# Kernel tuning notes

Measured on AMD Instinct MI355X. Metric: run time of the kernel, lower is better.

The kernel has to match this reference:

```python
import jax, jax.numpy as jnp
import numpy as np

B, T, D, E, FF, K = 4, 1024, 1024, 8, 2048, 2
SINKHORN_ITERS = 3


def setup_inputs() -> dict:
    key = jax.random.key(0)
    ks = jax.random.split(key, 7)
    scale = 0.02
    return {
        "x": jax.random.normal(ks[0], (B, T, D), dtype=jnp.float32),
        "router_w": jax.random.normal(ks[1], (E, D), dtype=jnp.float32) * scale,  # nn.Linear(D,E).weight
        "router_b": jnp.zeros((E,), dtype=jnp.float32),
        "temperature": jnp.ones((1,), dtype=jnp.float32) * 0.5,
        "wg": jax.random.normal(ks[2], (E, D, FF), dtype=jnp.float32) * scale,   # expert gate weights
        "wp": jax.random.normal(ks[3], (E, D, FF), dtype=jnp.float32) * scale,   # expert proj weights
        "wo": jax.random.normal(ks[4], (E, FF, D), dtype=jnp.float32) * scale,   # expert out_proj weights
    }


def _sinkhorn(log_alpha, iters=SINKHORN_ITERS):
    for _ in range(iters):
        log_alpha = log_alpha - jax.nn.logsumexp(log_alpha, axis=-1, keepdims=True)
        log_alpha = log_alpha - jax.nn.logsumexp(log_alpha, axis=-2, keepdims=True)
    gates = jnp.exp(log_alpha)
    return gates / (jnp.sum(gates, axis=-1, keepdims=True) + 1e-8)


def reference(x, router_w, router_b, temperature, wg, wp, wo):
    # Router scores with clamped temperature (clamp(min=0.1))
    temp = jnp.maximum(temperature, 0.1)
    scores = (jnp.einsum("btd,ed->bte", x, router_w) + router_b) / temp  # [B,T,E]

    # T>1 and E>1 -> Sinkhorn doubly-stochastic normalization
    gates = _sinkhorn(scores)

    topk_vals, topk_idx = jax.lax.top_k(gates, K)                 # [B,T,K]
    topk_gates = topk_vals / (jnp.sum(topk_vals, axis=-1, keepdims=True) + 1e-8)

    # Dense all-expert FFN (relu-gated GLU), matching mask-and-sum semantics.
    # sum_k sum_i (idx_k==i)*gate_k*expert_i(x) == sum_k gate_k * expert_{idx_k}(x)
    g = jax.nn.relu(jnp.einsum("btd,edf->btef", x, wg))           # [B,T,E,FF]
    p = jnp.einsum("btd,edf->btef", x, wp)                        # [B,T,E,FF]
    all_out = jnp.einsum("btef,efd->bted", g * p, wo)             # [B,T,E,D]

    gathered = jnp.take_along_axis(all_out, topk_idx[..., None], axis=2)  # [B,T,K,D]
    expert_out = jnp.sum(gathered * topk_gates[..., None], axis=2)        # [B,T,D]

    return x + expert_out
```

## Files before the change

kernel.cpp:

```cpp
#include <hip/hip_runtime.h>
#include <hip/hip_bf16.h>
#include <stdint.h>

#define B_   4
#define T_   1024
#define D_   1024
#define E_   8
#define FF_  2048
#define NT_  4096
#define LCAP 9216
#define NT1  (D_ / 32)
#define NT2  (FF_ / 32)

typedef unsigned short u16;
typedef __attribute__((ext_vector_type(8))) short bf16x8;
typedef __attribute__((ext_vector_type(4))) float f32x4;

#define MFMA16(a, b, c) __builtin_amdgcn_mfma_f32_16x16x32_bf16((a), (b), (c), 0, 0, 0)

__device__ __forceinline__ u16 f2bf(float f) {
  union { float f; uint32_t u; } c; c.f = f;
  return (u16)((c.u + 0x7FFFu + ((c.u >> 16) & 1u)) >> 16);
}

__device__ __forceinline__ void gl_lds16(const void* g, void* l) {
  __builtin_amdgcn_global_load_lds(
      (const __attribute__((address_space(1))) uint32_t*)g,
      (__attribute__((address_space(3))) uint32_t*)l, 16, 0, 0);
}


__global__ __launch_bounds__(256) void k_init(int* __restrict__ tok, float* __restrict__ gate,
                                              int* __restrict__ cnt, int* __restrict__ cur) {
  int i = blockIdx.x * 256 + threadIdx.x;
  if (i < LCAP) { tok[i] = 0; gate[i] = 0.f; }
  if (i < E_)   { cnt[i] = 0; cur[i] = 0; }
}

__global__ __launch_bounds__(256) void k_prep(const float4* __restrict__ x4,
                                              float4* __restrict__ out4,
                                              ushort4* __restrict__ xb4) {
  int i = blockIdx.x * 256 + threadIdx.x;
  float4 v = x4[i];
  out4[i] = v;
  ushort4 o; o.x = f2bf(v.x); o.y = f2bf(v.y); o.z = f2bf(v.z); o.w = f2bf(v.w);
  xb4[i] = o;
}

__global__ __launch_bounds__(256) void k_router(const float* __restrict__ x,
                                                const float* __restrict__ rw,
                                                const float* __restrict__ rb,
                                                const float* __restrict__ temp,
                                                float* __restrict__ scores) {
  int wid  = (blockIdx.x * 256 + threadIdx.x) >> 6;
  int lane = threadIdx.x & 63;
  const float* xr = x + (size_t)wid * D_;
  float acc[E_];
  #pragma unroll
  for (int e = 0; e < E_; ++e) acc[e] = 0.f;
  for (int i = lane; i < D_; i += 64) {
    float xv = xr[i];
    #pragma unroll
    for (int e = 0; e < E_; ++e) acc[e] += xv * rw[e * D_ + i];
  }
  float inv = 1.0f / fmaxf(temp[0], 0.1f);
  #pragma unroll
  for (int e = 0; e < E_; ++e) {
    float v = acc[e];
    for (int off = 32; off; off >>= 1) v += __shfl_xor(v, off);
    if (lane == 0) scores[(size_t)wid * E_ + e] = (v + rb[e]) * inv;
  }
}

__global__ __launch_bounds__(1024) void k_sinkhorn(const float* __restrict__ scores,
                                                   float* __restrict__ tkg, int* __restrict__ tki,
                                                   int* __restrict__ cnt) {
  const int b = blockIdx.x, t = threadIdx.x;
  const int row = b * T_ + t;
  float s[E_];
  #pragma unroll
  for (int e = 0; e < E_; ++e) s[e] = scores[(size_t)row * E_ + e];

  __shared__ float red[16][E_];
  __shared__ int lcnt[E_];
  if (t < E_) lcnt[t] = 0;
  const int wid = t >> 6, lane = t & 63;

  for (int it = 0; it < 3; ++it) {
    float m = s[0];
    #pragma unroll
    for (int e = 1; e < E_; ++e) m = fmaxf(m, s[e]);
    float sum = 0.f;
    #pragma unroll
    for (int e = 0; e < E_; ++e) sum += expf(s[e] - m);
    float lse = m + logf(sum);
    #pragma unroll
    for (int e = 0; e < E_; ++e) s[e] -= lse;

    float cm[E_];
    #pragma unroll
    for (int e = 0; e < E_; ++e) {
      float v = s[e];
      for (int off = 32; off; off >>= 1) v = fmaxf(v, __shfl_xor(v, off));
      if (lane == 0) red[wid][e] = v;
    }
    __syncthreads();
    #pragma unroll
    for (int e = 0; e < E_; ++e) {
      float mm = red[0][e];
      for (int wv = 1; wv < 16; ++wv) mm = fmaxf(mm, red[wv][e]);
      cm[e] = mm;
    }
    __syncthreads();
    #pragma unroll
    for (int e = 0; e < E_; ++e) {
      float v = expf(s[e] - cm[e]);
      for (int off = 32; off; off >>= 1) v += __shfl_xor(v, off);
      if (lane == 0) red[wid][e] = v;
    }
    __syncthreads();
    #pragma unroll
    for (int e = 0; e < E_; ++e) {
      float ss = 0.f;
      for (int wv = 0; wv < 16; ++wv) ss += red[wv][e];
      s[e] -= cm[e] + logf(ss);
    }
    __syncthreads();
  }

  float g[E_]; float rs = 0.f;
  #pragma unroll
  for (int e = 0; e < E_; ++e) { g[e] = expf(s[e]); rs += g[e]; }
  float inv = 1.f / (rs + 1e-8f);
  #pragma unroll
  for (int e = 0; e < E_; ++e) g[e] *= inv;

  int i0 = 0; float v0 = g[0];
  #pragma unroll
  for (int e = 1; e < E_; ++e) if (g[e] > v0) { v0 = g[e]; i0 = e; }
  int i1 = -1; float v1 = -1e30f;
  #pragma unroll
  for (int e = 0; e < E_; ++e) if (e != i0 && g[e] > v1) { v1 = g[e]; i1 = e; }
  float den = 1.f / (v0 + v1 + 1e-8f);
  tkg[row * 2 + 0] = v0 * den; tki[row * 2 + 0] = i0;
  tkg[row * 2 + 1] = v1 * den; tki[row * 2 + 1] = i1;

  atomicAdd(&lcnt[i0], 1);
  atomicAdd(&lcnt[i1], 1);
  __syncthreads();
  if (t < E_) atomicAdd(&cnt[t], lcnt[t]);
}

__global__ void k_offsets(const int* __restrict__ cnt, int* __restrict__ segoff) {
  if (threadIdx.x == 0 && blockIdx.x == 0) {
    int run = 0;
    for (int e = 0; e < E_; ++e) { segoff[e] = run; run += ((cnt[e] + 127) >> 7) << 7; }
  }
}

__global__ __launch_bounds__(256) void k_scatter(const int* __restrict__ tki, const float* __restrict__ tkg,
                                                 const int* __restrict__ segoff, int* __restrict__ cur,
                                                 int* __restrict__ tok, float* __restrict__ gate) {
  int idx = blockIdx.x * 256 + threadIdx.x;
  int row = idx >> 1;
  int e = tki[idx];
  float g = tkg[idx];
  int pos = atomicAdd(&cur[e], 1);
  int p = segoff[e] + pos;
  tok[p] = row;
  gate[p] = g;
}

__global__ __launch_bounds__(256) void k_transpose(const float* __restrict__ in, u16* __restrict__ out,
                                                   int R, int C) {
  __shared__ __align__(16) u16 t[32][36];
  const size_t msz = (size_t)R * C;
  const float* A = in + blockIdx.z * msz;
  u16* O = out + blockIdx.z * msz;
  const int r0 = blockIdx.y * 32, c0 = blockIdx.x * 32;
  const int tid = threadIdx.x;
  {
    const int i = tid >> 3, j4 = (tid & 7) << 2;
    const float4 v = *(const float4*)(A + (size_t)(r0 + i) * C + c0 + j4);
    ushort4 pk; pk.x = f2bf(v.x); pk.y = f2bf(v.y); pk.z = f2bf(v.z); pk.w = f2bf(v.w);
    *(ushort4*)(&t[i][j4]) = pk;
  }
  __syncthreads();
  {
    const int j2 = tid & 15;
    #pragma unroll
    for (int it = 0; it < 2; ++it) {
      const int r = (tid >> 4) + it * 16;
      uint32_t pv = (uint32_t)t[2 * j2][r] | ((uint32_t)t[2 * j2 + 1][r] << 16);
      *(uint32_t*)(O + (size_t)(c0 + r) * R + r0 + 2 * j2) = pv;
    }
  }
}


__global__ __launch_bounds__(512, 4) void k_stage1(
    const u16* __restrict__ wgT, const u16* __restrict__ wpT,
    const u16* __restrict__ xb, const int* __restrict__ tok,
    const int* __restrict__ cnt, const int* __restrict__ segoff,
    u16* __restrict__ H) {
  const int raw = blockIdx.x;
  const int e   = raw & 7;
  const int rem = raw >> 3;
  const int ft  = rem >> 5;
  const int pt  = rem & 31;
  if (pt * 128 >= cnt[e]) return;
  const int tid = threadIdx.x;
  const int lane = tid & 63;
  const int w = tid >> 6;
  const int lane15 = lane & 15, lchunk = lane >> 4;
  const int fw = w >> 2, pw = w & 3;

  __shared__ __align__(16) u16 LG[3][4096];
  __shared__ __align__(16) u16 LP[3][4096];
  __shared__ __align__(16) u16 LX[3][4096];

  const int prow0 = segoff[e] + pt * 128;
  const size_t wb = (size_t)e * FF_ * D_ + (size_t)(ft * 128 + w * 16 + lane15) * D_ + lchunk * 8;
  const u16* gsrc = wgT + wb;
  const u16* psrc = wpT + wb;
  const int tk = tok[prow0 + w * 16 + lane15];
  const u16* xsrc = xb + (size_t)tk * D_ + lchunk * 8;
  const int dstb = w * 512;

  const f32x4 vz = {0.f, 0.f, 0.f, 0.f};
  f32x4 accG[4][2], accP[4][2];
  #pragma unroll
  for (int m = 0; m < 4; ++m)
    #pragma unroll
    for (int n = 0; n < 2; ++n) { accG[m][n] = vz; accP[m][n] = vz; }

#define ISSUE1(c, t) do { const int o_ = (t) * 32;                 \
    gl_lds16(gsrc + o_, &LG[c][dstb]);                             \
    gl_lds16(psrc + o_, &LP[c][dstb]);                             \
    gl_lds16(xsrc + o_, &LX[c][dstb]); } while (0)

#define COMP1(c) do {                                                        \
    const u16* lg = LG[c]; const u16* lp = LP[c]; const u16* lx = LX[c];     \
    bf16x8 ag[4], ap[4], bx[2];                                              \
    _Pragma("unroll")                                                        \
    for (int m = 0; m < 4; ++m) {                                            \
      ag[m] = *(const bf16x8*)(lg + (fw * 4 + m) * 512 + lane * 8);          \
      ap[m] = *(const bf16x8*)(lp + (fw * 4 + m) * 512 + lane * 8);          \
    }                                                                        \
    _Pragma("unroll")                                                        \
    for (int n = 0; n < 2; ++n)                                              \
      bx[n] = *(const bf16x8*)(lx + (pw * 2 + n) * 512 + lane * 8);          \
    __builtin_amdgcn_s_setprio(1);                                           \
    _Pragma("unroll")                                                        \
    for (int m = 0; m < 4; ++m)                                              \
      _Pragma("unroll")                                                      \
      for (int n = 0; n < 2; ++n) {                                          \
        accG[m][n] = MFMA16(ag[m], bx[n], accG[m][n]);                       \
        accP[m][n] = MFMA16(ap[m], bx[n], accP[m][n]);                       \
      }                                                                      \
    __builtin_amdgcn_s_setprio(0); } while (0)

  ISSUE1(0, 0);
  ISSUE1(1, 1);
  #pragma unroll 1
  for (int t = 0; t < NT1 - 1; ++t) {
    asm volatile("s_waitcnt vmcnt(3)" ::: "memory");
    __builtin_amdgcn_s_barrier();
    asm volatile("" ::: "memory");
    if (t + 2 < NT1) { const int cn = (t + 2) % 3; ISSUE1(cn, t + 2); }
    const int c = t % 3;
    COMP1(c);
  }
  asm volatile("s_waitcnt vmcnt(0)" ::: "memory");
  __builtin_amdgcn_s_barrier();
  asm volatile("" ::: "memory");
  COMP1((NT1 - 1) % 3);
#undef ISSUE1
#undef COMP1

  const int jrow = lchunk * 4;
  #pragma unroll
  for (int m = 0; m < 4; ++m) {
    #pragma unroll
    for (int n = 0; n < 2; ++n) {
      union { uint2 v; u16 s[4]; } u;
      #pragma unroll
      for (int j = 0; j < 4; ++j)
        u.s[j] = f2bf(fmaxf(accG[m][n][j], 0.f) * accP[m][n][j]);
      const int prow = prow0 + pw * 32 + n * 16 + lane15;
      const int fcol = ft * 128 + fw * 64 + m * 16 + jrow;
      *(uint2*)(H + (size_t)prow * FF_ + fcol) = u.v;
    }
  }
}

__global__ __launch_bounds__(512, 4) void k_stage2(
    const u16* __restrict__ H, const u16* __restrict__ woT,
    const int* __restrict__ tok, const float* __restrict__ gate,
    const int* __restrict__ cnt, const int* __restrict__ segoff,
    float* __restrict__ out) {
  const int raw = blockIdx.x;
  const int e   = raw & 7;
  const int rem = raw >> 3;
  const int dt  = rem >> 5;
  const int pt  = rem & 31;
  if (pt * 128 >= cnt[e]) return;
  const int tid = threadIdx.x;
  const int lane = tid & 63;
  const int w = tid >> 6;
  const int lane15 = lane & 15, lchunk = lane >> 4;
  const int ph = w >> 2, dq = w & 3;

  __shared__ __align__(16) u16 LH[3][4096];
  __shared__ __align__(16) u16 LW[3][4096];
  __shared__ int   ltok[128];
  __shared__ float lgt[128];

  const int prow0 = segoff[e] + pt * 128;
  if (tid < 128) { ltok[tid] = tok[prow0 + tid]; lgt[tid] = gate[prow0 + tid]; }

  const u16* hsrc = H + (size_t)(prow0 + w * 16 + lane15) * FF_ + lchunk * 8;
  const u16* wsrc = woT + (size_t)e * D_ * FF_
                        + (size_t)(dt * 128 + w * 16 + lane15) * FF_ + lchunk * 8;
  const int dstb = w * 512;

  const f32x4 vz = {0.f, 0.f, 0.f, 0.f};
  f32x4 acc[4][2];
  #pragma unroll
  for (int m = 0; m < 4; ++m)
    #pragma unroll
    for (int n = 0; n < 2; ++n) acc[m][n] = vz;

#define ISSUE2(c, t) do { const int o_ = (t) * 32;                 \
    gl_lds16(hsrc + o_, &LH[c][dstb]);                             \
    gl_lds16(wsrc + o_, &LW[c][dstb]); } while (0)

#define COMP2(c) do {                                                        \
    const u16* lh = LH[c]; const u16* lw = LW[c];                            \
    bf16x8 ah[4], bw[2];                                                     \
    _Pragma("unroll")                                                        \
    for (int m = 0; m < 4; ++m)                                              \
      ah[m] = *(const bf16x8*)(lh + (ph * 4 + m) * 512 + lane * 8);          \
    _Pragma("unroll")                                                        \
    for (int n = 0; n < 2; ++n)                                              \
      bw[n] = *(const bf16x8*)(lw + (dq * 2 + n) * 512 + lane * 8);          \
    __builtin_amdgcn_s_setprio(1);                                           \
    _Pragma("unroll")                                                        \
    for (int m = 0; m < 4; ++m)                                              \
      _Pragma("unroll")                                                      \
      for (int n = 0; n < 2; ++n)                                            \
        acc[m][n] = MFMA16(ah[m], bw[n], acc[m][n]);                         \
    __builtin_amdgcn_s_setprio(0); } while (0)

  ISSUE2(0, 0);
  ISSUE2(1, 1);
  #pragma unroll 1
  for (int t = 0; t < NT2 - 1; ++t) {
    asm volatile("s_waitcnt vmcnt(2)" ::: "memory");
    __builtin_amdgcn_s_barrier();
    asm volatile("" ::: "memory");
    if (t + 2 < NT2) { const int cn = (t + 2) % 3; ISSUE2(cn, t + 2); }
    const int c = t % 3;
    COMP2(c);
  }
  asm volatile("s_waitcnt vmcnt(0)" ::: "memory");
  __builtin_amdgcn_s_barrier();
  asm volatile("" ::: "memory");
  COMP2((NT2 - 1) % 3);
#undef ISSUE2
#undef COMP2

  const int jrow = lchunk * 4;
  #pragma unroll
  for (int m = 0; m < 4; ++m) {
    #pragma unroll
    for (int n = 0; n < 2; ++n) {
      const int dcol = dt * 128 + dq * 32 + n * 16 + lane15;
      #pragma unroll
      for (int j = 0; j < 4; ++j) {
        const int pl = ph * 64 + m * 16 + jrow + j;
        unsafeAtomicAdd(&out[(size_t)ltok[pl] * D_ + dcol], lgt[pl] * acc[m][n][j]);
      }
    }
  }
}


extern "C" void kernel_launch(void* const* d_in, const int* in_sizes, int n_in,
                              void* d_out, int out_size, void* d_ws, size_t ws_size,
                              hipStream_t stream) {
  const float* x    = (const float*)d_in[0];
  const float* rw   = (const float*)d_in[1];
  const float* rb   = (const float*)d_in[2];
  const float* temp = (const float*)d_in[3];
  const float* wg   = (const float*)d_in[4];
  const float* wp   = (const float*)d_in[5];
  const float* wo   = (const float*)d_in[6];
  float* out = (float*)d_out;
  char* ws = (char*)d_ws;

  const size_t O_XB  = 0;
  const size_t O_WGT = 8388608;
  const size_t O_WPT = O_WGT + 33554432;
  const size_t O_WOT = O_WGT;
  const size_t O_H   = O_WPT + 33554432;
  const size_t O_SC  = O_H + (size_t)LCAP * FF_ * 2;
  const size_t O_TKG = O_SC + (size_t)NT_ * E_ * 4;
  const size_t O_TKI = O_TKG + (size_t)NT_ * 2 * 4;
  const size_t O_CNT = O_TKI + (size_t)NT_ * 2 * 4;
  const size_t O_CUR = O_CNT + 128;
  const size_t O_SEG = O_CUR + 128;
  const size_t O_TOK = O_SEG + 128;
  const size_t O_GTE = O_TOK + (size_t)LCAP * 4;
  const size_t REQ   = O_GTE + (size_t)LCAP * 4;
  if (ws_size < REQ) return;

  u16*   xb     = (u16*)(ws + O_XB);
  u16*   wgT    = (u16*)(ws + O_WGT);
  u16*   wpT    = (u16*)(ws + O_WPT);
  u16*   woT    = (u16*)(ws + O_WOT);
  u16*   Hbuf   = (u16*)(ws + O_H);
  float* scores = (float*)(ws + O_SC);
  float* tkg    = (float*)(ws + O_TKG);
  int*   tki    = (int*)(ws + O_TKI);
  int*   cnt    = (int*)(ws + O_CNT);
  int*   cur    = (int*)(ws + O_CUR);
  int*   segoff = (int*)(ws + O_SEG);
  int*   tok    = (int*)(ws + O_TOK);
  float* gate   = (float*)(ws + O_GTE);

  k_init<<<(LCAP + 255) / 256, 256, 0, stream>>>(tok, gate, cnt, cur);
  k_prep<<<(NT_ * D_ / 4) / 256, 256, 0, stream>>>((const float4*)x, (float4*)out, (ushort4*)xb);
  k_router<<<NT_ / 4, 256, 0, stream>>>(x, rw, rb, temp, scores);
  k_sinkhorn<<<B_, 1024, 0, stream>>>(scores, tkg, tki, cnt);
  k_offsets<<<1, 64, 0, stream>>>(cnt, segoff);
  k_scatter<<<(NT_ * 2) / 256, 256, 0, stream>>>(tki, tkg, segoff, cur, tok, gate);

  k_transpose<<<dim3(FF_ / 32, D_ / 32, E_), 256, 0, stream>>>(wg, wgT, D_, FF_);
  k_transpose<<<dim3(FF_ / 32, D_ / 32, E_), 256, 0, stream>>>(wp, wpT, D_, FF_);

  k_stage1<<<32 * 16 * E_, 512, 0, stream>>>(wgT, wpT, xb, tok, cnt, segoff, Hbuf);

  k_transpose<<<dim3(D_ / 32, FF_ / 32, E_), 256, 0, stream>>>(wo, woT, FF_, D_);

  k_stage2<<<32 * 8 * E_, 512, 0, stream>>>(Hbuf, woT, tok, gate, cnt, segoff, out);
}
```

Baseline: 479.2 us.

## Interleave gate/proj weights and enlarge stage1 tiles to 256x256 with K=64 steps

Gate and proj weights are transposed into one interleaved buffer, so stage1 computes a single 256(F-pair)x256(token) tile per block with larger per-wave accumulators. It double-buffers K=64 chunks and staggers the next-chunk loads between MFMA phases. This raises reuse of each loaded operand and cuts LDS traffic per MFMA. The x copy/bf16 cast is also fused into the router kernel, removing one launch and one pass over x. In exchange the block count halves, occupancy drops to 2 blocks per CU, register pressure rises, and segment padding can waste more work, which a bounds check on segend only partly offsets for output stores.

New measurement: 471.4 us. Within noise of the previous version (-1.6%).

```diff
diff --git a/kernel.cpp b/kernel.cpp
--- a/kernel.cpp
+++ b/kernel.cpp
@@ -8,8 +8,8 @@
 #define E_   8
 #define FF_  2048
 #define NT_  4096
-#define LCAP 9216
-#define NT1  (D_ / 32)
+#define LCAP 9472
+#define NTS1 (D_ / 64)
 #define NT2  (FF_ / 32)
 
 typedef unsigned short u16;
@@ -37,29 +37,25 @@
   if (i < E_)   { cnt[i] = 0; cur[i] = 0; }
 }
 
-__global__ __launch_bounds__(256) void k_prep(const float4* __restrict__ x4,
-                                              float4* __restrict__ out4,
-                                              ushort4* __restrict__ xb4) {
-  int i = blockIdx.x * 256 + threadIdx.x;
-  float4 v = x4[i];
-  out4[i] = v;
-  ushort4 o; o.x = f2bf(v.x); o.y = f2bf(v.y); o.z = f2bf(v.z); o.w = f2bf(v.w);
-  xb4[i] = o;
-}
-
 __global__ __launch_bounds__(256) void k_router(const float* __restrict__ x,
                                                 const float* __restrict__ rw,
                                                 const float* __restrict__ rb,
                                                 const float* __restrict__ temp,
-                                                float* __restrict__ scores) {
+                                                float* __restrict__ scores,
+                                                float* __restrict__ out,
+                                                u16* __restrict__ xb) {
   int wid  = (blockIdx.x * 256 + threadIdx.x) >> 6;
   int lane = threadIdx.x & 63;
   const float* xr = x + (size_t)wid * D_;
+  float* orow = out + (size_t)wid * D_;
+  u16* xrow = xb + (size_t)wid * D_;
   float acc[E_];
   #pragma unroll
   for (int e = 0; e < E_; ++e) acc[e] = 0.f;
   for (int i = lane; i < D_; i += 64) {
     float xv = xr[i];
+    orow[i] = xv;
+    xrow[i] = f2bf(xv);
     #pragma unroll
     for (int e = 0; e < E_; ++e) acc[e] += xv * rw[e * D_ + i];
   }
@@ -155,6 +151,7 @@
   if (threadIdx.x == 0 && blockIdx.x == 0) {
     int run = 0;
     for (int e = 0; e < E_; ++e) { segoff[e] = run; run += ((cnt[e] + 127) >> 7) << 7; }
+    segoff[E_] = run;
   }
 }
 
@@ -197,99 +194,140 @@
   }
 }
 
-
-__global__ __launch_bounds__(512, 4) void k_stage1(
-    const u16* __restrict__ wgT, const u16* __restrict__ wpT,
-    const u16* __restrict__ xb, const int* __restrict__ tok,
-    const int* __restrict__ cnt, const int* __restrict__ segoff,
+__global__ __launch_bounds__(256) void k_transpose_w(const float* __restrict__ in,
+                                                     u16* __restrict__ out, int woff) {
+  __shared__ __align__(16) u16 t[32][36];
+  const float* A = in + (size_t)blockIdx.z * D_ * FF_;
+  u16* O = out + (size_t)blockIdx.z * 4096 * 1024;
+  const int r0 = blockIdx.y * 32, c0 = blockIdx.x * 32;
+  const int tid = threadIdx.x;
+  {
+    const int i = tid >> 3, j4 = (tid & 7) << 2;
+    const float4 v = *(const float4*)(A + (size_t)(r0 + i) * FF_ + c0 + j4);
+    ushort4 pk; pk.x = f2bf(v.x); pk.y = f2bf(v.y); pk.z = f2bf(v.z); pk.w = f2bf(v.w);
+    *(ushort4*)(&t[i][j4]) = pk;
+  }
+  __syncthreads();
+  {
+    const int j2 = tid & 15;
+    #pragma unroll
+    for (int it = 0; it < 2; ++it) {
+      const int r = (tid >> 4) + it * 16;
+      const int f = c0 + r;
+      const int fp = ((f >> 4) << 5) + (f & 15) + woff;
+      uint32_t pv = (uint32_t)t[2 * j2][r] | ((uint32_t)t[2 * j2 + 1][r] << 16);
+      *(uint32_t*)(O + (size_t)fp * 1024 + r0 + 2 * j2) = pv;
+    }
+  }
+}
+
+
+__global__ __launch_bounds__(512, 2) void k_stage1(
+    const u16* __restrict__ wa, const u16* __restrict__ xb,
+    const int* __restrict__ tok, const int* __restrict__ segoff,
     u16* __restrict__ H) {
   const int raw = blockIdx.x;
   const int e   = raw & 7;
   const int rem = raw >> 3;
-  const int ft  = rem >> 5;
-  const int pt  = rem & 31;
-  if (pt * 128 >= cnt[e]) return;
+  const int ft  = rem >> 4;
+  const int pt2 = rem & 15;
+  const int seg0 = segoff[e], segend = segoff[e + 1];
+  if (pt2 * 256 >= segend - seg0) return;
   const int tid = threadIdx.x;
   const int lane = tid & 63;
   const int w = tid >> 6;
   const int lane15 = lane & 15, lchunk = lane >> 4;
+  const int lk8 = lchunk * 8;
   const int fw = w >> 2, pw = w & 3;
 
-  __shared__ __align__(16) u16 LG[3][4096];
-  __shared__ __align__(16) u16 LP[3][4096];
-  __shared__ __align__(16) u16 LX[3][4096];
-
-  const int prow0 = segoff[e] + pt * 128;
-  const size_t wb = (size_t)e * FF_ * D_ + (size_t)(ft * 128 + w * 16 + lane15) * D_ + lchunk * 8;
-  const u16* gsrc = wgT + wb;
-  const u16* psrc = wpT + wb;
-  const int tk = tok[prow0 + w * 16 + lane15];
-  const u16* xsrc = xb + (size_t)tk * D_ + lchunk * 8;
-  const int dstb = w * 512;
+  __shared__ __align__(16) u16 LA[2][16384];
+  __shared__ __align__(16) u16 LB[2][16384];
+
+  const int prow0 = seg0 + pt2 * 256;
+  const u16* asrc0 = wa + (size_t)e * 4096 * 1024
+                        + (size_t)(ft * 256 + 2 * w * 16 + lane15) * 1024 + lk8;
+  const u16* asrc1 = asrc0 + 16 * 1024;
+  const int tk0 = tok[prow0 + 2 * w * 16 + lane15];
+  const int tk1 = tok[prow0 + 2 * w * 16 + 16 + lane15];
+  const u16* bsrc0 = xb + (size_t)tk0 * D_ + lk8;
+  const u16* bsrc1 = xb + (size_t)tk1 * D_ + lk8;
+  const int dA0 = 2 * w * 512, dA1 = dA0 + 512;
 
   const f32x4 vz = {0.f, 0.f, 0.f, 0.f};
-  f32x4 accG[4][2], accP[4][2];
-  #pragma unroll
-  for (int m = 0; m < 4; ++m)
-    #pragma unroll
-    for (int n = 0; n < 2; ++n) { accG[m][n] = vz; accP[m][n] = vz; }
-
-#define ISSUE1(c, t) do { const int o_ = (t) * 32;                 \
-    gl_lds16(gsrc + o_, &LG[c][dstb]);                             \
-    gl_lds16(psrc + o_, &LP[c][dstb]);                             \
-    gl_lds16(xsrc + o_, &LX[c][dstb]); } while (0)
-
-#define COMP1(c) do {                                                        \
-    const u16* lg = LG[c]; const u16* lp = LP[c]; const u16* lx = LX[c];     \
-    bf16x8 ag[4], ap[4], bx[2];                                              \
-    _Pragma("unroll")                                                        \
-    for (int m = 0; m < 4; ++m) {                                            \
-      ag[m] = *(const bf16x8*)(lg + (fw * 4 + m) * 512 + lane * 8);          \
-      ap[m] = *(const bf16x8*)(lp + (fw * 4 + m) * 512 + lane * 8);          \
-    }                                                                        \
-    _Pragma("unroll")                                                        \
-    for (int n = 0; n < 2; ++n)                                              \
-      bx[n] = *(const bf16x8*)(lx + (pw * 2 + n) * 512 + lane * 8);          \
-    __builtin_amdgcn_s_setprio(1);                                           \
-    _Pragma("unroll")                                                        \
-    for (int m = 0; m < 4; ++m)                                              \
-      _Pragma("unroll")                                                      \
-      for (int n = 0; n < 2; ++n) {                                          \
-        accG[m][n] = MFMA16(ag[m], bx[n], accG[m][n]);                       \
-        accP[m][n] = MFMA16(ap[m], bx[n], accP[m][n]);                       \
-      }                                                                      \
-    __builtin_amdgcn_s_setprio(0); } while (0)
-
-  ISSUE1(0, 0);
-  ISSUE1(1, 1);
+  f32x4 acc[8][4];
+  #pragma unroll
+  for (int m = 0; m < 8; ++m)
+    #pragma unroll
+    for (int n = 0; n < 4; ++n) acc[m][n] = vz;
+
+#define STG_A(c, s) do { const int o_ = (s) * 64;           \
+    gl_lds16(asrc0 + o_,      &LA[c][dA0]);                 \
+    gl_lds16(asrc0 + o_ + 32, &LA[c][dA0 + 8192]);          \
+    gl_lds16(asrc1 + o_,      &LA[c][dA1]);                 \
+    gl_lds16(asrc1 + o_ + 32, &LA[c][dA1 + 8192]); } while (0)
+#define STG_B(c, s) do { const int o_ = (s) * 64;           \
+    gl_lds16(bsrc0 + o_,      &LB[c][dA0]);                 \
+    gl_lds16(bsrc0 + o_ + 32, &LB[c][dA0 + 8192]);          \
+    gl_lds16(bsrc1 + o_,      &LB[c][dA1]);                 \
+    gl_lds16(bsrc1 + o_ + 32, &LB[c][dA1 + 8192]); } while (0)
+
+  STG_A(0, 0); STG_B(0, 0);
   #pragma unroll 1
-  for (int t = 0; t < NT1 - 1; ++t) {
-    asm volatile("s_waitcnt vmcnt(3)" ::: "memory");
+  for (int s = 0; s < NTS1; ++s) {
+    const int c = s & 1;
+    asm volatile("s_waitcnt vmcnt(0)" ::: "memory");
     __builtin_amdgcn_s_barrier();
     asm volatile("" ::: "memory");
-    if (t + 2 < NT1) { const int cn = (t + 2) % 3; ISSUE1(cn, t + 2); }
-    const int c = t % 3;
-    COMP1(c);
-  }
-  asm volatile("s_waitcnt vmcnt(0)" ::: "memory");
-  __builtin_amdgcn_s_barrier();
-  asm volatile("" ::: "memory");
-  COMP1((NT1 - 1) % 3);
-#undef ISSUE1
-#undef COMP1
+    const u16* la = LA[c];
+    const u16* lb = LB[c];
+    bf16x8 bv[4][2];
+    #pragma unroll
+    for (int n = 0; n < 4; ++n)
+      #pragma unroll
+      for (int kc = 0; kc < 2; ++kc)
+        bv[n][kc] = *(const bf16x8*)(lb + kc * 8192 + (pw * 4 + n) * 512 + lane * 8);
+    #pragma unroll
+    for (int p = 0; p < 4; ++p) {
+      bf16x8 av[2][2];
+      #pragma unroll
+      for (int mm = 0; mm < 2; ++mm)
+        #pragma unroll
+        for (int kc = 0; kc < 2; ++kc)
+          av[mm][kc] = *(const bf16x8*)(la + kc * 8192 + (fw * 8 + 2 * p + mm) * 512 + lane * 8);
+      if (p == 0) { if (s + 1 < NTS1) STG_A(c ^ 1, s + 1); }
+      if (p == 1) { if (s + 1 < NTS1) STG_B(c ^ 1, s + 1); }
+      __builtin_amdgcn_s_setprio(1);
+      #pragma unroll
+      for (int mm = 0; mm < 2; ++mm)
+        #pragma unroll
+        for (int n = 0; n < 4; ++n)
+          #pragma unroll
+          for (int kc = 0; kc < 2; ++kc)
+            acc[2 * p + mm][n] = MFMA16(av[mm][kc], bv[n][kc], acc[2 * p + mm][n]);
+      __builtin_amdgcn_s_setprio(0);
+      if (p < 3) {
+        __builtin_amdgcn_s_barrier();
+        asm volatile("" ::: "memory");
+      }
+    }
+  }
+#undef STG_A
+#undef STG_B
 
   const int jrow = lchunk * 4;
   #pragma unroll
-  for (int m = 0; m < 4; ++m) {
-    #pragma unroll
-    for (int n = 0; n < 2; ++n) {
-      union { uint2 v; u16 s[4]; } u;
-      #pragma unroll
-      for (int j = 0; j < 4; ++j)
-        u.s[j] = f2bf(fmaxf(accG[m][n][j], 0.f) * accP[m][n][j]);
-      const int prow = prow0 + pw * 32 + n * 16 + lane15;
-      const int fcol = ft * 128 + fw * 64 + m * 16 + jrow;
-      *(uint2*)(H + (size_t)prow * FF_ + fcol) = u.v;
+  for (int q = 0; q < 4; ++q) {
+    const int fcol = ft * 128 + fw * 64 + q * 16 + jrow;
+    #pragma unroll
+    for (int n = 0; n < 4; ++n) {
+      const int prow = prow0 + pw * 64 + n * 16 + lane15;
+      if (prow < segend) {
+        union { uint2 v; u16 s[4]; } u;
+        #pragma unroll
+        for (int j = 0; j < 4; ++j)
+          u.s[j] = f2bf(fmaxf(acc[2 * q][n][j], 0.f) * acc[2 * q + 1][n][j]);
+        *(uint2*)(H + (size_t)prow * FF_ + fcol) = u.v;
+      }
     }
   }
 }
@@ -400,10 +438,9 @@
   char* ws = (char*)d_ws;
 
   const size_t O_XB  = 0;
-  const size_t O_WGT = 8388608;
-  const size_t O_WPT = O_WGT + 33554432;
-  const size_t O_WOT = O_WGT;
-  const size_t O_H   = O_WPT + 33554432;
+  const size_t O_WA  = 8388608;
+  const size_t O_WOT = O_WA;
+  const size_t O_H   = O_WA + 67108864;
   const size_t O_SC  = O_H + (size_t)LCAP * FF_ * 2;
   const size_t O_TKG = O_SC + (size_t)NT_ * E_ * 4;
   const size_t O_TKI = O_TKG + (size_t)NT_ * 2 * 4;
@@ -416,8 +453,7 @@
   if (ws_size < REQ) return;
 
   u16*   xb     = (u16*)(ws + O_XB);
-  u16*   wgT    = (u16*)(ws + O_WGT);
-  u16*   wpT    = (u16*)(ws + O_WPT);
+  u16*   wa     = (u16*)(ws + O_WA);
   u16*   woT    = (u16*)(ws + O_WOT);
   u16*   Hbuf   = (u16*)(ws + O_H);
   float* scores = (float*)(ws + O_SC);
@@ -430,16 +466,15 @@
   float* gate   = (float*)(ws + O_GTE);
 
   k_init<<<(LCAP + 255) / 256, 256, 0, stream>>>(tok, gate, cnt, cur);
-  k_prep<<<(NT_ * D_ / 4) / 256, 256, 0, stream>>>((const float4*)x, (float4*)out, (ushort4*)xb);
-  k_router<<<NT_ / 4, 256, 0, stream>>>(x, rw, rb, temp, scores);
+  k_router<<<NT_ / 4, 256, 0, stream>>>(x, rw, rb, temp, scores, out, xb);
   k_sinkhorn<<<B_, 1024, 0, stream>>>(scores, tkg, tki, cnt);
   k_offsets<<<1, 64, 0, stream>>>(cnt, segoff);
   k_scatter<<<(NT_ * 2) / 256, 256, 0, stream>>>(tki, tkg, segoff, cur, tok, gate);
 
-  k_transpose<<<dim3(FF_ / 32, D_ / 32, E_), 256, 0, stream>>>(wg, wgT, D_, FF_);
-  k_transpose<<<dim3(FF_ / 32, D_ / 32, E_), 256, 0, stream>>>(wp, wpT, D_, FF_);
-
-  k_stage1<<<32 * 16 * E_, 512, 0, stream>>>(wgT, wpT, xb, tok, cnt, segoff, Hbuf);
+  k_transpose_w<<<dim3(FF_ / 32, D_ / 32, E_), 256, 0, stream>>>(wg, wa, 0);
+  k_transpose_w<<<dim3(FF_ / 32, D_ / 32, E_), 256, 0, stream>>>(wp, wa, 16);
+
+  k_stage1<<<16 * 16 * E_, 512, 0, stream>>>(wa, xb, tok, segoff, Hbuf);
 
   k_transpose<<<dim3(D_ / 32, FF_ / 32, E_), 256, 0, stream>>>(wo, woT, FF_, D_);
 
```
